# Optimization experiments

Measured on AMD Instinct MI355X. Metric: run time of the kernel, lower is better.

## Reference

```python
import jax, jax.numpy as jnp
import numpy as np

HIDDEN = 768
INTER = 3072
HEADS = 12
HEAD_DIM = INTER // HEADS  # 256
LN_EPS = 1e-6
R_SOFTPLUS_0 = 1.442695041


def setup_inputs() -> dict:
    key = jax.random.key(0)
    ks = jax.random.split(key, 12)
    s = 0.02
    inp = {
        "hidden_states": jax.random.normal(ks[0], (8, 4096, HIDDEN), dtype=jnp.float32),
        "pooling_query": jax.random.normal(ks[1], (1, 1, HIDDEN), dtype=jnp.float32) * s,
        "Wq": jax.random.normal(ks[2], (HIDDEN, INTER), dtype=jnp.float32) * s,
        "bq": jnp.zeros((INTER,), dtype=jnp.float32),
        "Wk": jax.random.normal(ks[3], (HIDDEN, INTER), dtype=jnp.float32) * s,
        "bk": jnp.zeros((INTER,), dtype=jnp.float32),
        "Wv": jax.random.normal(ks[4], (HIDDEN, INTER), dtype=jnp.float32) * s,
        "bv": jnp.zeros((INTER,), dtype=jnp.float32),
        "Wp": jax.random.normal(ks[5], (INTER, HIDDEN), dtype=jnp.float32) * s,
        "bp": jnp.zeros((HIDDEN,), dtype=jnp.float32),
        "per_dim_scale": jnp.zeros((HEAD_DIM,), dtype=jnp.float32),
        "ln_w": jnp.ones((HIDDEN,), dtype=jnp.float32),
        "ln_b": jnp.zeros((HIDDEN,), dtype=jnp.float32),
    }
    return inp


def reference(hidden_states, pooling_query, Wq, bq, Wk, bk, Wv, bv, Wp, bp,
              per_dim_scale, ln_w, ln_b):
    B, S, _ = hidden_states.shape
    dt = hidden_states.dtype

    # Query: single pooling token, identical across batch -> [H, D]
    q = (pooling_query.reshape(1, HIDDEN) @ Wq + bq).reshape(HEADS, HEAD_DIM)
    # PerDimScale: q * (r_softplus0/sqrt(D)) * softplus(per_dim_scale)
    scale = (R_SOFTPLUS_0 / np.sqrt(HEAD_DIM)).astype(np.float32)
    q = q * (scale * jax.nn.softplus(per_dim_scale))

    # K/V projections: [B, S, H, D]
    k = (hidden_states @ Wk + bk).reshape(B, S, HEADS, HEAD_DIM)
    v = (hidden_states @ Wv + bv).reshape(B, S, HEADS, HEAD_DIM)

    # Single-query attention: logits [B, H, S]; scaling=1.0 (scale_logits_by_head_dims=False)
    # logit cap skipped (no_attention_logit_cap=True)
    logits = jnp.einsum("hd,bshd->bhs", q, k)
    attn = jax.nn.softmax(logits.astype(jnp.float32), axis=-1).astype(dt)

    # Weighted sum over seq: [B, H, D] -> concat heads -> [B, H*D]
    ctx = jnp.einsum("bhs,bshd->bhd", attn, v).reshape(B, HEADS * HEAD_DIM)

    out = ctx @ Wp + bp  # [B, HIDDEN]
    # LayerNorm; note the original forward adds ones to ln weight in-place each call,
    # so effective weight for one call is (ln_w + 1).
    mean = jnp.mean(out, axis=-1, keepdims=True)
    var = jnp.var(out, axis=-1, keepdims=True)
    out = (out - mean) * jax.lax.rsqrt(var + LN_EPS) * (ln_w + 1.0) + ln_b

    pooled = out[:, None, :]  # [B, 1, HIDDEN]
    attn_weights = attn[:, :, None, :]  # [B, H, 1, S]
    return pooled, attn_weights
```

## Files before the change

kernel.cpp:

```cpp
#include <hip/hip_runtime.h>
#include <cstdint>
#include <cmath>

#define LN_EPS 1e-6f

#define N_QCH 24u
#define O_QPART 0u
#define O_Q     73728u
#define O_WK    76800u
#define O_BKE   86016u
#define O_PHP   86032u
#define N_SC    32
#define O_PH    (O_PHP + 2359296u)
#define O_CTXP  (O_PH + 73728u)
#define N_CCH   12
#define O_CTX   (O_CTXP + 294912u)
#define O_OUTP  (O_CTX + 24576u)
#define N_ICH   48

__device__ __forceinline__ float waveReduceSum(float v) {
#pragma unroll
    for (int o = 32; o >= 1; o >>= 1) v += __shfl_xor(v, o, 64);
    return v;
}
__device__ __forceinline__ float waveReduceMax(float v) {
#pragma unroll
    for (int o = 32; o >= 1; o >>= 1) v = fmaxf(v, __shfl_xor(v, o, 64));
    return v;
}

__global__ __launch_bounds__(256) void k1_qpart(const float* __restrict__ pq,
                                                const float* __restrict__ Wq,
                                                float* __restrict__ ws) {
    int h = blockIdx.x % 12;
    int ch = blockIdx.x / 12;
    int tid = threadIdx.x;
    int col = h * 256 + tid;
    int c0 = ch * 32;
    float acc = 0.f;
#pragma unroll 8
    for (int i = 0; i < 32; ++i) {
        int c = c0 + i;
        acc += pq[c] * Wq[c * 3072 + col];
    }
    ws[O_QPART + ch * 3072 + col] = acc;
}

__global__ __launch_bounds__(256) void k1b_qreduce(const float* __restrict__ bq,
                                                   const float* __restrict__ pds,
                                                   float* __restrict__ ws) {
    int j = blockIdx.x * 256 + threadIdx.x;
    float acc = bq[j];
#pragma unroll
    for (unsigned ch = 0; ch < N_QCH; ++ch) acc += ws[O_QPART + ch * 3072 + j];
    float x = pds[j & 255];
    float sp = (x > 20.f) ? x : log1pf(expf(x));
    const float scale = 1.442695041f / 16.0f;
    ws[O_Q + j] = acc * scale * sp;
}

__global__ __launch_bounds__(256) void k2_wkeff(const float* __restrict__ Wk,
                                                const float* __restrict__ bk,
                                                float* __restrict__ ws) {
    __shared__ float sh[4];
    int tid = threadIdx.x;
    int blk = blockIdx.x;
    float v;
    if (blk < 9216) {
        int c = blk / 12, h = blk % 12;
        v = Wk[c * 3072 + h * 256 + tid] * ws[O_Q + h * 256 + tid];
    } else {
        int h = blk - 9216;
        v = bk[h * 256 + tid] * ws[O_Q + h * 256 + tid];
    }
    v = waveReduceSum(v);
    if ((tid & 63) == 0) sh[tid >> 6] = v;
    __syncthreads();
    if (tid == 0) {
        float s = sh[0] + sh[1] + sh[2] + sh[3];
        if (blk < 9216) {
            int c = blk / 12, h = blk % 12;
            ws[O_WK + c * 12 + h] = s;
        } else {
            ws[O_BKE + (blk - 9216)] = s;
        }
    }
}

__global__ __launch_bounds__(256) void k3_logits(const float* __restrict__ hidden,
                                                 const float* __restrict__ ws,
                                                 float* __restrict__ attn) {
    __shared__ float tile[192 * 65];
    __shared__ float red[48 * 64];
    int blk = blockIdx.x;
    int b = blk >> 6;
    int s0 = (blk & 63) * 64;
    const float* hb = hidden + (size_t)(b * 4096 + s0) * 768;
    int tid = threadIdx.x;
    int w = tid >> 6, lane = tid & 63;
    float acc[12];
#pragma unroll
    for (int h = 0; h < 12; ++h) acc[h] = 0.f;
    const float* wk = ws + O_WK;
    for (int ch = 0; ch < 4; ++ch) {
        int cbase = ch * 192;
        __syncthreads();
#pragma unroll
        for (int it = 0; it < 12; ++it) {
            int idx = it * 256 + tid;
            int r = idx / 48, cc4 = idx % 48;
            const float4 v = *reinterpret_cast<const float4*>(hb + r * 768 + cbase + cc4 * 4);
            int c0 = cc4 * 4;
            tile[(c0 + 0) * 65 + r] = v.x;
            tile[(c0 + 1) * 65 + r] = v.y;
            tile[(c0 + 2) * 65 + r] = v.z;
            tile[(c0 + 3) * 65 + r] = v.w;
        }
        __syncthreads();
#pragma unroll 4
        for (int j = 0; j < 48; ++j) {
            int cc = w * 48 + j;
            float x = tile[cc * 65 + lane];
            const float4* wr = reinterpret_cast<const float4*>(wk + (cbase + cc) * 12);
            float4 w0 = wr[0], w1 = wr[1], w2 = wr[2];
            acc[0] += x * w0.x;  acc[1] += x * w0.y;  acc[2]  += x * w0.z;  acc[3]  += x * w0.w;
            acc[4] += x * w1.x;  acc[5] += x * w1.y;  acc[6]  += x * w1.z;  acc[7]  += x * w1.w;
            acc[8] += x * w2.x;  acc[9] += x * w2.y;  acc[10] += x * w2.z;  acc[11] += x * w2.w;
        }
    }
    __syncthreads();
#pragma unroll
    for (int h = 0; h < 12; ++h) red[(w * 12 + h) * 64 + lane] = acc[h];
    __syncthreads();
    const float* bke = ws + O_BKE;
    for (int idx = tid; idx < 768; idx += 256) {
        int h = idx / 64, r = idx & 63;
        float v = red[(0 + h) * 64 + r] + red[(12 + h) * 64 + r] +
                  red[(24 + h) * 64 + r] + red[(36 + h) * 64 + r] + bke[h];
        attn[(size_t)(b * 12 + h) * 4096 + s0 + r] = v;
    }
}

__global__ __launch_bounds__(256) void k4_softmax(float* __restrict__ attn) {
    __shared__ float sh[4];
    int row = blockIdx.x;
    float* base = attn + (size_t)row * 4096;
    int tid = threadIdx.x;
    float4 x[4];
#pragma unroll
    for (int t = 0; t < 4; ++t) x[t] = reinterpret_cast<float4*>(base)[t * 256 + tid];
    float m = -1e30f;
#pragma unroll
    for (int t = 0; t < 4; ++t) {
        m = fmaxf(m, fmaxf(fmaxf(x[t].x, x[t].y), fmaxf(x[t].z, x[t].w)));
    }
    m = waveReduceMax(m);
    if ((tid & 63) == 0) sh[tid >> 6] = m;
    __syncthreads();
    m = fmaxf(fmaxf(sh[0], sh[1]), fmaxf(sh[2], sh[3]));
    __syncthreads();
    float s = 0.f;
#pragma unroll
    for (int t = 0; t < 4; ++t) {
        x[t].x = expf(x[t].x - m); x[t].y = expf(x[t].y - m);
        x[t].z = expf(x[t].z - m); x[t].w = expf(x[t].w - m);
        s += x[t].x + x[t].y + x[t].z + x[t].w;
    }
    s = waveReduceSum(s);
    if ((tid & 63) == 0) sh[tid >> 6] = s;
    __syncthreads();
    s = sh[0] + sh[1] + sh[2] + sh[3];
    float inv = 1.0f / s;
#pragma unroll
    for (int t = 0; t < 4; ++t) {
        x[t].x *= inv; x[t].y *= inv; x[t].z *= inv; x[t].w *= inv;
        reinterpret_cast<float4*>(base)[t * 256 + tid] = x[t];
    }
}

__global__ __launch_bounds__(256) void k5_phpart(const float* __restrict__ hidden,
                                                 const float* __restrict__ attn,
                                                 float* __restrict__ ws) {
    int blk = blockIdx.x;
    int sc = blk & 31;
    int ct = (blk >> 5) % 3;
    int b = blk / 96;
    int tid = threadIdx.x;
    int c = ct * 256 + tid;
    int s0 = sc * 128;
    const float* hb = hidden + (size_t)(b * 4096 + s0) * 768 + c;
    const float* ab = attn + (size_t)b * 49152 + s0;
    float acc[12];
#pragma unroll
    for (int h = 0; h < 12; ++h) acc[h] = 0.f;
    for (int g = 0; g < 32; ++g) {
        float x0 = hb[(g * 4 + 0) * 768];
        float x1 = hb[(g * 4 + 1) * 768];
        float x2 = hb[(g * 4 + 2) * 768];
        float x3 = hb[(g * 4 + 3) * 768];
#pragma unroll
        for (int h = 0; h < 12; ++h) {
            const float4 a = *reinterpret_cast<const float4*>(ab + h * 4096 + g * 4);
            acc[h] += a.x * x0 + a.y * x1 + a.z * x2 + a.w * x3;
        }
    }
    float* php = ws + O_PHP;
#pragma unroll
    for (int h = 0; h < 12; ++h)
        php[(size_t)(sc * 96 + b * 12 + h) * 768 + c] = acc[h];
}

__global__ __launch_bounds__(256) void k6_phreduce(float* __restrict__ ws) {
    int gid = blockIdx.x * 256 + threadIdx.x;
    const float* php = ws + O_PHP;
    float s = 0.f;
#pragma unroll
    for (int sc = 0; sc < N_SC; ++sc) s += php[(size_t)sc * 73728 + gid];
    ws[O_PH + gid] = s;
}

__global__ __launch_bounds__(256) void k7_ctxpart(const float* __restrict__ Wv,
                                                  float* __restrict__ ws) {
    int blk = blockIdx.x;
    int jt = blk % 12, cch = blk / 12;
    int tid = threadIdx.x;
    int j = jt * 256 + tid;
    int h = jt;
    const float* ph = ws + O_PH;
    float acc[8];
#pragma unroll
    for (int b = 0; b < 8; ++b) acc[b] = 0.f;
    for (int cc = 0; cc < 64; ++cc) {
        int c = cch * 64 + cc;
        float wv = Wv[(size_t)c * 3072 + j];
#pragma unroll
        for (int b = 0; b < 8; ++b) acc[b] += ph[(b * 12 + h) * 768 + c] * wv;
    }
#pragma unroll
    for (int b = 0; b < 8; ++b)
        ws[O_CTXP + (size_t)(cch * 8 + b) * 3072 + j] = acc[b];
}

__global__ __launch_bounds__(256) void k7b_ctxreduce(const float* __restrict__ bv,
                                                     float* __restrict__ ws) {
    int gid = blockIdx.x * 256 + threadIdx.x;
    int b = gid / 3072, i = gid % 3072;
    float s = bv[i];
#pragma unroll
    for (int cch = 0; cch < N_CCH; ++cch) s += ws[O_CTXP + (size_t)(cch * 8 + b) * 3072 + i];
    ws[O_CTX + gid] = s;
}

__global__ __launch_bounds__(256) void k8_outpart(const float* __restrict__ Wp,
                                                  float* __restrict__ ws) {
    int blk = blockIdx.x;
    int jt = blk % 3, ich = blk / 3;
    int tid = threadIdx.x;
    int j = jt * 256 + tid;
    const float* ctx = ws + O_CTX;
    float acc[8];
#pragma unroll
    for (int b = 0; b < 8; ++b) acc[b] = 0.f;
    for (int ii = 0; ii < 64; ++ii) {
        int i = ich * 64 + ii;
        float wp = Wp[(size_t)i * 768 + j];
#pragma unroll
        for (int b = 0; b < 8; ++b) acc[b] += ctx[b * 3072 + i] * wp;
    }
#pragma unroll
    for (int b = 0; b < 8; ++b)
        ws[O_OUTP + (size_t)(ich * 8 + b) * 768 + j] = acc[b];
}

__global__ __launch_bounds__(256) void k9_ln(const float* __restrict__ bp,
                                             const float* __restrict__ ln_w,
                                             const float* __restrict__ ln_b,
                                             const float* __restrict__ ws,
                                             float* __restrict__ pooled) {
    __shared__ float sh[8];
    int b = blockIdx.x, tid = threadIdx.x;
    const float* op = ws + O_OUTP;
    float vals[3];
    float lsum = 0.f, lsq = 0.f;
#pragma unroll
    for (int t = 0; t < 3; ++t) {
        int j = t * 256 + tid;
        float v = bp[j];
#pragma unroll
        for (int ich = 0; ich < N_ICH; ++ich) v += op[(size_t)(ich * 8 + b) * 768 + j];
        vals[t] = v; lsum += v; lsq += v * v;
    }
    lsum = waveReduceSum(lsum);
    lsq = waveReduceSum(lsq);
    if ((tid & 63) == 0) { sh[tid >> 6] = lsum; sh[4 + (tid >> 6)] = lsq; }
    __syncthreads();
    float mean = (sh[0] + sh[1] + sh[2] + sh[3]) * (1.f / 768.f);
    float var = (sh[4] + sh[5] + sh[6] + sh[7]) * (1.f / 768.f) - mean * mean;
    float inv = rsqrtf(var + LN_EPS);
#pragma unroll
    for (int t = 0; t < 3; ++t) {
        int j = t * 256 + tid;
        pooled[b * 768 + j] = (vals[t] - mean) * inv * (ln_w[j] + 1.f) + ln_b[j];
    }
}

extern "C" void kernel_launch(void* const* d_in, const int* in_sizes, int n_in,
                              void* d_out, int out_size, void* d_ws, size_t ws_size,
                              hipStream_t stream) {
    const float* hidden = (const float*)d_in[0];
    const float* pq     = (const float*)d_in[1];
    const float* Wq     = (const float*)d_in[2];
    const float* bq     = (const float*)d_in[3];
    const float* Wk     = (const float*)d_in[4];
    const float* bk     = (const float*)d_in[5];
    const float* Wv     = (const float*)d_in[6];
    const float* bv     = (const float*)d_in[7];
    const float* Wp     = (const float*)d_in[8];
    const float* bp     = (const float*)d_in[9];
    const float* pds    = (const float*)d_in[10];
    const float* ln_w   = (const float*)d_in[11];
    const float* ln_b   = (const float*)d_in[12];
    float* out = (float*)d_out;
    float* ws  = (float*)d_ws;
    float* pooled = out;
    float* attn   = out + 6144;

    k1_qpart   <<<288, 256, 0, stream>>>(pq, Wq, ws);
    k1b_qreduce<<<12, 256, 0, stream>>>(bq, pds, ws);
    k2_wkeff   <<<9228, 256, 0, stream>>>(Wk, bk, ws);
    k3_logits  <<<512, 256, 0, stream>>>(hidden, ws, attn);
    k4_softmax <<<96, 256, 0, stream>>>(attn);
    k5_phpart  <<<768, 256, 0, stream>>>(hidden, attn, ws);
    k6_phreduce<<<288, 256, 0, stream>>>(ws);
    k7_ctxpart <<<144, 256, 0, stream>>>(Wv, ws);
    k7b_ctxreduce<<<96, 256, 0, stream>>>(bv, ws);
    k8_outpart <<<144, 256, 0, stream>>>(Wp, ws);
    k9_ln      <<<8, 256, 0, stream>>>(bp, ln_w, ln_b, ws, pooled);
}
```

Baseline: 291.9 us.

## Split logits kernel over hidden halves, swizzle LDS tile, drop key-bias term

The logits kernel now splits the 768-wide reduction into two halves across twice as many blocks. It writes partial logits to workspace, and the softmax kernel sums the two halves as it loads them. The hidden tile is stored as XOR-swizzled float4 rows instead of a padded transposed scalar tile, and the effective key weights are staged in LDS rather than read from global memory. The per-head key-bias term is removed, since adding a constant per head does not change the softmax. The cost is an extra partial-logit round trip through workspace.

```diff
diff --git a/kernel.cpp b/kernel.cpp
--- a/kernel.cpp
+++ b/kernel.cpp
@@ -10,6 +10,7 @@
 #define O_WK    76800u
 #define O_BKE   86016u
 #define O_PHP   86032u
+#define O_PLOG  O_PHP
 #define N_SC    32
 #define O_PH    (O_PHP + 2359296u)
 #define O_CTXP  (O_PH + 73728u)
@@ -60,95 +61,90 @@
 }
 
 __global__ __launch_bounds__(256) void k2_wkeff(const float* __restrict__ Wk,
-                                                const float* __restrict__ bk,
                                                 float* __restrict__ ws) {
     __shared__ float sh[4];
     int tid = threadIdx.x;
     int blk = blockIdx.x;
-    float v;
-    if (blk < 9216) {
-        int c = blk / 12, h = blk % 12;
-        v = Wk[c * 3072 + h * 256 + tid] * ws[O_Q + h * 256 + tid];
-    } else {
-        int h = blk - 9216;
-        v = bk[h * 256 + tid] * ws[O_Q + h * 256 + tid];
-    }
+    int c = blk / 12, h = blk % 12;
+    float v = Wk[c * 3072 + h * 256 + tid] * ws[O_Q + h * 256 + tid];
     v = waveReduceSum(v);
     if ((tid & 63) == 0) sh[tid >> 6] = v;
     __syncthreads();
-    if (tid == 0) {
-        float s = sh[0] + sh[1] + sh[2] + sh[3];
-        if (blk < 9216) {
-            int c = blk / 12, h = blk % 12;
-            ws[O_WK + c * 12 + h] = s;
-        } else {
-            ws[O_BKE + (blk - 9216)] = s;
-        }
-    }
+    if (tid == 0) ws[O_WK + c * 12 + h] = sh[0] + sh[1] + sh[2] + sh[3];
 }
 
 __global__ __launch_bounds__(256) void k3_logits(const float* __restrict__ hidden,
-                                                 const float* __restrict__ ws,
-                                                 float* __restrict__ attn) {
-    __shared__ float tile[192 * 65];
-    __shared__ float red[48 * 64];
-    int blk = blockIdx.x;
-    int b = blk >> 6;
-    int s0 = (blk & 63) * 64;
+                                                 float* __restrict__ ws) {
+    __shared__ float4 tile4[1536];
+    __shared__ float4 wkb4[288];
+    int blk = blockIdx.x;
+    int half = blk & 1;
+    int st = (blk >> 1) & 63;
+    int b = blk >> 7;
+    int s0 = st * 64;
     const float* hb = hidden + (size_t)(b * 4096 + s0) * 768;
+    const float4* wkg4 = reinterpret_cast<const float4*>(ws + O_WK);
     int tid = threadIdx.x;
     int w = tid >> 6, lane = tid & 63;
     float acc[12];
 #pragma unroll
     for (int h = 0; h < 12; ++h) acc[h] = 0.f;
-    const float* wk = ws + O_WK;
+
     for (int ch = 0; ch < 4; ++ch) {
-        int cbase = ch * 192;
+        int cbase = half * 384 + ch * 96;
         __syncthreads();
-#pragma unroll
-        for (int it = 0; it < 12; ++it) {
+        for (int i = tid; i < 288; i += 256) wkb4[i] = wkg4[cbase * 3 + i];
+#pragma unroll
+        for (int it = 0; it < 6; ++it) {
             int idx = it * 256 + tid;
-            int r = idx / 48, cc4 = idx % 48;
-            const float4 v = *reinterpret_cast<const float4*>(hb + r * 768 + cbase + cc4 * 4);
-            int c0 = cc4 * 4;
-            tile[(c0 + 0) * 65 + r] = v.x;
-            tile[(c0 + 1) * 65 + r] = v.y;
-            tile[(c0 + 2) * 65 + r] = v.z;
-            tile[(c0 + 3) * 65 + r] = v.w;
+            int r = idx / 24, j = idx % 24;
+            const float4 v = *reinterpret_cast<const float4*>(hb + r * 768 + cbase + j * 4);
+            tile4[r * 24 + (j ^ (r & 7))] = v;
         }
         __syncthreads();
-#pragma unroll 4
-        for (int j = 0; j < 48; ++j) {
-            int cc = w * 48 + j;
-            float x = tile[cc * 65 + lane];
-            const float4* wr = reinterpret_cast<const float4*>(wk + (cbase + cc) * 12);
-            float4 w0 = wr[0], w1 = wr[1], w2 = wr[2];
-            acc[0] += x * w0.x;  acc[1] += x * w0.y;  acc[2]  += x * w0.z;  acc[3]  += x * w0.w;
-            acc[4] += x * w1.x;  acc[5] += x * w1.y;  acc[6]  += x * w1.z;  acc[7]  += x * w1.w;
-            acc[8] += x * w2.x;  acc[9] += x * w2.y;  acc[10] += x * w2.z;  acc[11] += x * w2.w;
+#pragma unroll
+        for (int jj = 0; jj < 6; ++jj) {
+            int jcol = w * 6 + jj;
+            float4 x = tile4[lane * 24 + (jcol ^ (lane & 7))];
+            const float4* wr = &wkb4[jcol * 12];
+            float xc[4] = {x.x, x.y, x.z, x.w};
+#pragma unroll
+            for (int cc = 0; cc < 4; ++cc) {
+                float4 w0 = wr[cc * 3 + 0], w1 = wr[cc * 3 + 1], w2 = wr[cc * 3 + 2];
+                acc[0] += xc[cc] * w0.x;  acc[1] += xc[cc] * w0.y;  acc[2]  += xc[cc] * w0.z;  acc[3]  += xc[cc] * w0.w;
+                acc[4] += xc[cc] * w1.x;  acc[5] += xc[cc] * w1.y;  acc[6]  += xc[cc] * w1.z;  acc[7]  += xc[cc] * w1.w;
+                acc[8] += xc[cc] * w2.x;  acc[9] += xc[cc] * w2.y;  acc[10] += xc[cc] * w2.z;  acc[11] += xc[cc] * w2.w;
+            }
         }
     }
     __syncthreads();
+    float* red = reinterpret_cast<float*>(tile4);
 #pragma unroll
     for (int h = 0; h < 12; ++h) red[(w * 12 + h) * 64 + lane] = acc[h];
     __syncthreads();
-    const float* bke = ws + O_BKE;
+    float* plog = ws + O_PLOG;
     for (int idx = tid; idx < 768; idx += 256) {
         int h = idx / 64, r = idx & 63;
         float v = red[(0 + h) * 64 + r] + red[(12 + h) * 64 + r] +
-                  red[(24 + h) * 64 + r] + red[(36 + h) * 64 + r] + bke[h];
-        attn[(size_t)(b * 12 + h) * 4096 + s0 + r] = v;
-    }
-}
-
-__global__ __launch_bounds__(256) void k4_softmax(float* __restrict__ attn) {
+                  red[(24 + h) * 64 + r] + red[(36 + h) * 64 + r];
+        plog[(size_t)half * 393216 + (size_t)(b * 12 + h) * 4096 + s0 + r] = v;
+    }
+}
+
+__global__ __launch_bounds__(256) void k4_softmax(const float* __restrict__ ws,
+                                                  float* __restrict__ attn) {
     __shared__ float sh[4];
     int row = blockIdx.x;
+    const float4* p0 = reinterpret_cast<const float4*>(ws + O_PLOG + (size_t)row * 4096);
+    const float4* p1 = reinterpret_cast<const float4*>(ws + O_PLOG + 393216u + (size_t)row * 4096);
     float* base = attn + (size_t)row * 4096;
     int tid = threadIdx.x;
     float4 x[4];
 #pragma unroll
-    for (int t = 0; t < 4; ++t) x[t] = reinterpret_cast<float4*>(base)[t * 256 + tid];
+    for (int t = 0; t < 4; ++t) {
+        float4 a = p0[t * 256 + tid], c = p1[t * 256 + tid];
+        x[t].x = a.x + c.x; x[t].y = a.y + c.y; x[t].z = a.z + c.z; x[t].w = a.w + c.w;
+    }
     float m = -1e30f;
 #pragma unroll
     for (int t = 0; t < 4; ++t) {
@@ -312,9 +308,8 @@
     const float* Wq     = (const float*)d_in[2];
     const float* bq     = (const float*)d_in[3];
     const float* Wk     = (const float*)d_in[4];
-    const float* bk     = (const float*)d_in[5];
+    const float* bv     = (const float*)d_in[7];
     const float* Wv     = (const float*)d_in[6];
-    const float* bv     = (const float*)d_in[7];
     const float* Wp     = (const float*)d_in[8];
     const float* bp     = (const float*)d_in[9];
     const float* pds    = (const float*)d_in[10];
@@ -327,9 +322,9 @@
 
     k1_qpart   <<<288, 256, 0, stream>>>(pq, Wq, ws);
     k1b_qreduce<<<12, 256, 0, stream>>>(bq, pds, ws);
-    k2_wkeff   <<<9228, 256, 0, stream>>>(Wk, bk, ws);
-    k3_logits  <<<512, 256, 0, stream>>>(hidden, ws, attn);
-    k4_softmax <<<96, 256, 0, stream>>>(attn);
+    k2_wkeff   <<<9216, 256, 0, stream>>>(Wk, ws);
+    k3_logits  <<<1024, 256, 0, stream>>>(hidden, ws);
+    k4_softmax <<<96, 256, 0, stream>>>(ws, attn);
     k5_phpart  <<<768, 256, 0, stream>>>(hidden, attn, ws);
     k6_phreduce<<<288, 256, 0, stream>>>(ws);
     k7_ctxpart <<<144, 256, 0, stream>>>(Wv, ws);
```

Measured after the change: 273.2 us. 1.07x faster.
